# Performance work log

Measured on AMD Instinct MI355X. Metric: run time of the kernel, lower is better.

The kernel has to match this reference:

```python
import jax, jax.numpy as jnp
import numpy as np

N, E, G = 20000, 320000, 64
DIN, H, EF, FC, OUT = 128, 256, 16, 256, 1
BN_EPS = 1e-5


def _gine_layer(x, src, dst, edge_attr, We, be, Wa, ba, g, bt, Wb, bb):
    # GINEConv (eps=0): out = mlp(x + sum_j relu(x_j + lin_edge(e_ij)))
    e = edge_attr @ We.T + be                      # [E, in_ch]
    m = jax.nn.relu(x[src] + e)                    # messages [E, in_ch]
    agg = jax.ops.segment_sum(m, dst, num_segments=x.shape[0])
    h = (x + agg) @ Wa.T + ba                      # Linear
    # BatchNorm1d in eval mode with running_mean=0, running_var=1
    inv = jax.lax.rsqrt(jnp.asarray(1.0 + BN_EPS, h.dtype))
    h = jax.nn.relu(h * inv * g + bt)
    return jax.nn.relu(h @ Wb.T + bb)


def _mean_pool(h, batch, num_graphs):
    sums = jax.ops.segment_sum(h, batch, num_segments=num_graphs)
    cnt = jax.ops.segment_sum(jnp.ones((h.shape[0],), h.dtype), batch, num_segments=num_graphs)
    return sums / jnp.maximum(cnt, 1.0)[:, None]


def setup_inputs() -> dict:
    key = jax.random.key(0)
    ks = iter(jax.random.split(key, 64))

    def nrm(shape, s=0.05):
        return jax.random.normal(next(ks), shape, jnp.float32) * s

    inp = {
        "x": jax.random.normal(next(ks), (N, DIN), jnp.float32),
        "edge_attr": jax.random.normal(next(ks), (E, EF), jnp.float32),
        "src": jax.random.randint(next(ks), (E,), 0, N),
        "dst": jax.random.randint(next(ks), (E,), 0, N),
        "batch": jnp.sort(jax.random.randint(next(ks), (N,), 0, G)),
    }
    dims = [(DIN, H), (H, H), (H, H)]
    for i, (din, h) in enumerate(dims, start=1):
        inp[f"We{i}"] = nrm((din, EF));  inp[f"be{i}"] = jnp.zeros((din,), jnp.float32)
        inp[f"Wa{i}"] = nrm((h, din));  inp[f"ba{i}"] = jnp.zeros((h,), jnp.float32)
        inp[f"g{i}"] = jnp.ones((h,), jnp.float32); inp[f"bt{i}"] = jnp.zeros((h,), jnp.float32)
        inp[f"Wb{i}"] = nrm((h, h));    inp[f"bb{i}"] = jnp.zeros((h,), jnp.float32)
    inp["L1w"] = nrm((FC * 3, H * 3)); inp["L1b"] = jnp.zeros((FC * 3,), jnp.float32)
    inp["L2w"] = nrm((OUT, FC * 3));   inp["L2b"] = jnp.zeros((OUT,), jnp.float32)
    return inp


def reference(x, edge_attr, src, dst, batch,
              We1, be1, Wa1, ba1, g1, bt1, Wb1, bb1,
              We2, be2, Wa2, ba2, g2, bt2, Wb2, bb2,
              We3, be3, Wa3, ba3, g3, bt3, Wb3, bb3,
              L1w, L1b, L2w, L2b):
    h1 = _gine_layer(x,  src, dst, edge_attr, We1, be1, Wa1, ba1, g1, bt1, Wb1, bb1)
    h2 = _gine_layer(h1, src, dst, edge_attr, We2, be2, Wa2, ba2, g2, bt2, Wb2, bb2)
    h3 = _gine_layer(h2, src, dst, edge_attr, We3, be3, Wa3, ba3, g3, bt3, Wb3, bb3)
    p = jnp.concatenate([_mean_pool(h1, batch, G),
                         _mean_pool(h2, batch, G),
                         _mean_pool(h3, batch, G)], axis=1)   # [G, 3H]
    h = jax.nn.relu(p @ L1w.T + L1b)   # dropout is identity (training=False)
    return jax.nn.sigmoid(h @ L2w.T + L2b)
```

## Files before the change

kernel.cpp:

```cpp
#include <hip/hip_runtime.h>
#include <math.h>
#include <stdint.h>

#define N_NODES 20000
#define M_PAD 20032
#define N_EDGES 320000
#define N_GRAPHS 64
#define DIN 128
#define H 256
#define POOL_W 768
#define CHUNK 40
#define NCHUNK (N_EDGES / CHUNK)

typedef __attribute__((ext_vector_type(8))) short bf16x8;
typedef __attribute__((ext_vector_type(4))) float f32x4;
typedef __attribute__((ext_vector_type(4))) unsigned int u32x4;
typedef __attribute__((ext_vector_type(2))) unsigned int u32x2;
typedef _Float16 h2 __attribute__((ext_vector_type(2)));

__device__ __forceinline__ unsigned short f2bf(float f) {
    unsigned u = __builtin_bit_cast(unsigned, f);
    u += 0x7FFFu + ((u >> 16) & 1u);
    return (unsigned short)(u >> 16);
}
__device__ __forceinline__ float bf2f(unsigned short u) {
    return __builtin_bit_cast(float, (unsigned)u << 16);
}
__device__ __forceinline__ unsigned short f2h(float f) {
    const _Float16 h = (_Float16)f;
    return __builtin_bit_cast(unsigned short, h);
}

#if __has_builtin(__builtin_amdgcn_fdot2)
#define DOT2(a, b, c) __builtin_amdgcn_fdot2((a), (b), (c), false)
#else
__device__ __forceinline__ float dot2_fallback(h2 a, h2 b, float c) {
    return fmaf((float)a.x, (float)b.x, fmaf((float)a.y, (float)b.y, c));
}
#define DOT2(a, b, c) dot2_fallback((a), (b), (c))
#endif

struct CvtJob  { const float* s; unsigned short* d; int n4; int mode; };
struct CvtJobs { CvtJob j[12]; };

__global__ __launch_bounds__(256) void cvt_all(CvtJobs jobs)
{
    const CvtJob J = jobs.j[blockIdx.y];
    if (J.mode == 2) {
        const ushort4 z = {0, 0, 0, 0};
        for (int i = blockIdx.x * 256 + threadIdx.x; i < J.n4; i += gridDim.x * 256)
            ((ushort4*)J.d)[i] = z;
        return;
    }
    if (J.mode == 1) {
        for (int i = blockIdx.x * 256 + threadIdx.x; i < J.n4; i += gridDim.x * 256) {
            const float4 v = ((const float4*)J.s)[i];
            ushort4 r;
            r.x = f2h(v.x); r.y = f2h(v.y); r.z = f2h(v.z); r.w = f2h(v.w);
            ((ushort4*)J.d)[i] = r;
        }
        return;
    }
    for (int i = blockIdx.x * 256 + threadIdx.x; i < J.n4; i += gridDim.x * 256) {
        const float4 v = ((const float4*)J.s)[i];
        ushort4 r;
        r.x = f2bf(v.x); r.y = f2bf(v.y); r.z = f2bf(v.z); r.w = f2bf(v.w);
        ((ushort4*)J.d)[i] = r;
    }
}

__global__ __launch_bounds__(256) void hist_kernel(const int* __restrict__ dst,
                                                   int* __restrict__ deg)
{
    const int i = blockIdx.x * 256 + threadIdx.x;
    if (i < N_EDGES) atomicAdd(deg + dst[i], 1);
}

__global__ __launch_bounds__(1024) void scan_kernel(const int* __restrict__ deg,
                                                    int* __restrict__ off,
                                                    int* __restrict__ cur,
                                                    const int* __restrict__ batch,
                                                    int* __restrict__ start)
{
    __shared__ int wsum[16];
    __shared__ int carry;
    const int tid = threadIdx.x, wave = tid >> 6, lane = tid & 63;
    if (tid == 0) carry = 0;
    __syncthreads();
    for (int base = 0; base < N_NODES; base += 1024) {
        const int i = base + tid;
        const int v = (i < N_NODES) ? deg[i] : 0;
        int s = v;
#pragma unroll
        for (int d = 1; d < 64; d <<= 1) {
            const int t = __shfl_up(s, d);
            if (lane >= d) s += t;
        }
        if (lane == 63) wsum[wave] = s;
        __syncthreads();
        if (wave == 0) {
            int t = (lane < 16) ? wsum[lane] : 0;
#pragma unroll
            for (int d = 1; d < 16; d <<= 1) {
                const int u = __shfl_up(t, d);
                if (lane >= d) t += u;
            }
            if (lane < 16) wsum[lane] = t;
        }
        __syncthreads();
        const int wbase = (wave == 0) ? 0 : wsum[wave - 1];
        if (i < N_NODES) {
            const int o = carry + wbase + s - v;
            off[i] = o;
            cur[i] = o;
        }
        const int tot = wsum[15];
        __syncthreads();
        if (tid == 0) carry += tot;
        __syncthreads();
    }
    if (tid == 0) off[N_NODES] = carry;

    if (tid <= N_GRAPHS) {
        if (tid == N_GRAPHS) { start[N_GRAPHS] = N_NODES; }
        else {
            int lo = 0, hi = N_NODES;
            while (lo < hi) { const int mid = (lo + hi) >> 1; if (batch[mid] < tid) lo = mid + 1; else hi = mid; }
            start[tid] = lo;
        }
    }
}

__global__ __launch_bounds__(256) void chunkmap_kernel(const int* __restrict__ off,
                                                       int* __restrict__ cmap)
{
    const int w = blockIdx.x * 256 + threadIdx.x;
    if (w > NCHUNK) return;
    if (w == NCHUNK) { cmap[w] = N_NODES; return; }
    const int target = w * CHUNK;
    int lo = 0, hi = N_NODES;
    while (lo < hi) { const int mid = (lo + hi) >> 1; if (off[mid] < target) lo = mid + 1; else hi = mid; }
    cmap[w] = lo;
}

__global__ __launch_bounds__(256) void scatter_kernel(
    const int* __restrict__ src, const int* __restrict__ dst,
    const float* __restrict__ ea, int* __restrict__ cursor,
    int* __restrict__ ssrc, unsigned short* __restrict__ eas)
{
    const int e = blockIdx.x * 256 + threadIdx.x;
    if (e < N_EDGES) {
        const int p = atomicAdd(cursor + dst[e], 1);
        ssrc[p] = src[e];
        const float4* er = (const float4*)(ea + (size_t)e * 16);
        unsigned short* dr = eas + (size_t)p * 16;
        ushort4* d4 = (ushort4*)dr;
#pragma unroll
        for (int q = 0; q < 4; ++q) {
            const float4 v = er[q];
            ushort4 r;
            r.x = f2h(v.x); r.y = f2h(v.y); r.z = f2h(v.z); r.w = f2h(v.w);
            d4[q] = r;
        }
    }
}

template<int IN>
__global__ __launch_bounds__(256) void agg3(
    const unsigned short* __restrict__ xb,
    const unsigned short* __restrict__ eas,
    const int* __restrict__ ssrc,
    const int* __restrict__ off,
    const int* __restrict__ cmap,
    const unsigned short* __restrict__ Weh,
    const float* __restrict__ be,
    unsigned short* __restrict__ out)
{
    constexpr int CPL = IN / 64;
    constexpr int XW  = CPL / 2;
    const int lane = threadIdx.x & 63;
    const int wid  = blockIdx.x * 4 + (threadIdx.x >> 6);
    const int c0 = lane * CPL;
    const int zd = __builtin_amdgcn_mbcnt_lo(0u, 0u);

    u32x4 wlo[CPL], whi[CPL];
    float bias[CPL], acc[CPL];
#pragma unroll
    for (int j = 0; j < CPL; ++j) {
        const u32x4* wr = (const u32x4*)(Weh + (size_t)(c0 + j) * 16);
        wlo[j] = wr[0];
        whi[j] = wr[1];
        bias[j] = be[c0 + j];
        acc[j]  = 0.0f;
    }
#pragma unroll
    for (int j = 0; j < CPL; ++j) {
#pragma unroll
        for (int k = 0; k < 4; ++k) {
            { float t = __builtin_bit_cast(float, wlo[j][k]); asm volatile("" : "+v"(t)); wlo[j][k] = __builtin_bit_cast(unsigned int, t); }
            { float t = __builtin_bit_cast(float, whi[j][k]); asm volatile("" : "+v"(t)); whi[j][k] = __builtin_bit_cast(unsigned int, t); }
        }
        asm volatile("" : "+v"(bias[j]));
    }

    int n          = __builtin_amdgcn_readfirstlane(cmap[wid]);
    const int nend = __builtin_amdgcn_readfirstlane(cmap[wid + 1]);
    if (n >= nend) return;
    int p          = __builtin_amdgcn_readfirstlane(off[n]);
    const int pend = __builtin_amdgcn_readfirstlane(off[nend]);

    auto ldx = [&](int s) -> u32x2 {
        if constexpr (XW == 2) {
            return *(const u32x2*)(xb + (size_t)s * IN + c0);
        } else {
            u32x2 r;
            r[0] = *(const unsigned int*)(xb + (size_t)s * IN + c0);
            r[1] = 0u;
            return r;
        }
    };
    auto flushv = [&](int nn, u32x2 xs) {
        if constexpr (XW == 2) {
            const float x0 = __builtin_bit_cast(float, xs[0] << 16);
            const float x1 = __builtin_bit_cast(float, xs[0] & 0xFFFF0000u);
            const float x2 = __builtin_bit_cast(float, xs[1] << 16);
            const float x3 = __builtin_bit_cast(float, xs[1] & 0xFFFF0000u);
            u32x2 o;
            o[0] = (unsigned)f2bf(x0 + acc[0]) | ((unsigned)f2bf(x1 + acc[1]) << 16);
            o[1] = (unsigned)f2bf(x2 + acc[2]) | ((unsigned)f2bf(x3 + acc[3]) << 16);
            *(u32x2*)(out + (size_t)nn * IN + c0) = o;
        } else {
            const float x0 = __builtin_bit_cast(float, xs[0] << 16);
            const float x1 = __builtin_bit_cast(float, xs[0] & 0xFFFF0000u);
            const unsigned int o =
                (unsigned)f2bf(x0 + acc[0]) | ((unsigned)f2bf(x1 + acc[1]) << 16);
            *(unsigned int*)(out + (size_t)nn * IN + c0) = o;
        }
#pragma unroll
        for (int j = 0; j < CPL; ++j) acc[j] = 0.0f;
    };

    int p1 = __builtin_amdgcn_readfirstlane(off[n + 1]);
    while (p1 == p) {
        flushv(n, ldx(n)); ++n;
        if (n >= nend) return;
        p1 = __builtin_amdgcn_readfirstlane(off[n + 1]);
    }
    u32x2 xself = ldx(n);

    auto ldeL = [&](int q) -> u32x4 {
        return ((const u32x4*)(eas + (size_t)(q + zd) * 16))[0];
    };
    auto ldeH = [&](int q) -> u32x4 {
        return ((const u32x4*)(eas + (size_t)(q + zd) * 16))[1];
    };
    auto ldsrc = [&](int q) -> int {
        const int qc = (q < N_EDGES) ? q : (N_EDGES - 1);
        return ssrc[qc + zd];
    };
    auto edge_compute = [&](u32x4 eL, u32x4 eH, u32x2 xw) {
        float m[CPL];
#pragma unroll
        for (int j = 0; j < CPL; ++j) m[j] = bias[j];
#pragma unroll
        for (int k = 0; k < 4; ++k) {
            const h2 ep = __builtin_bit_cast(h2, eL[k]);
#pragma unroll
            for (int j = 0; j < CPL; ++j)
                m[j] = DOT2(ep, __builtin_bit_cast(h2, wlo[j][k]), m[j]);
        }
#pragma unroll
        for (int k = 0; k < 4; ++k) {
            const h2 ep = __builtin_bit_cast(h2, eH[k]);
#pragma unroll
            for (int j = 0; j < CPL; ++j)
                m[j] = DOT2(ep, __builtin_bit_cast(h2, whi[j][k]), m[j]);
        }
#pragma unroll
        for (int j = 0; j < CPL; ++j) {
            const unsigned int word = xw[j >> 1];
            const float xf = __builtin_bit_cast(float,
                (j & 1) ? (word & 0xFFFF0000u) : (word << 16));
            acc[j] += fmaxf(m[j] + xf, 0.0f);
        }
    };
    auto adv = [&]() {
        flushv(n, xself); ++n;
        while (n < nend) {
            p1 = __builtin_amdgcn_readfirstlane(off[n + 1]);
            if (p1 != p) { xself = ldx(n); break; }
            flushv(n, ldx(n)); ++n;
        }
    };

    int sA = ldsrc(p),     sB = ldsrc(p + 1), sC = ldsrc(p + 2), sD = ldsrc(p + 3);
    u32x4 eLA = ldeL(p),     eHA = ldeH(p);
    u32x4 eLB = ldeL(p + 1), eHB = ldeH(p + 1);
    u32x4 eLC = ldeL(p + 2), eHC = ldeH(p + 2);
    u32x4 eLD = ldeL(p + 3), eHD = ldeH(p + 3);
    u32x2 xA = ldx(sA), xB = ldx(sB), xC = ldx(sC), xD = ldx(sD);
    sA = ldsrc(p + 4); sB = ldsrc(p + 5); sC = ldsrc(p + 6); sD = ldsrc(p + 7);

    for (;;) {
        edge_compute(eLA, eHA, xA);
        eLA = ldeL(p + 4); eHA = ldeH(p + 4); xA = ldx(sA); sA = ldsrc(p + 8);
        ++p; if (p == p1) adv();
        if (p >= pend) break;

        edge_compute(eLB, eHB, xB);
        eLB = ldeL(p + 4); eHB = ldeH(p + 4); xB = ldx(sB); sB = ldsrc(p + 8);
        ++p; if (p == p1) adv();
        if (p >= pend) break;

        edge_compute(eLC, eHC, xC);
        eLC = ldeL(p + 4); eHC = ldeH(p + 4); xC = ldx(sC); sC = ldsrc(p + 8);
        ++p; if (p == p1) adv();
        if (p >= pend) break;

        edge_compute(eLD, eHD, xD);
        eLD = ldeL(p + 4); eHD = ldeH(p + 4); xD = ldx(sD); sD = ldsrc(p + 8);
        ++p; if (p == p1) adv();
        if (p >= pend) break;
    }
    while (n < nend) { flushv(n, ldx(n)); ++n; }
}

template<int K, int EPI>
__global__ __launch_bounds__(256) void gemm_ldsA(
    const unsigned short* __restrict__ A,
    const unsigned short* __restrict__ W,
    const float* __restrict__ bias,
    const float* __restrict__ gsc, const float* __restrict__ bsh,
    unsigned short* __restrict__ out)
{
    constexpr int KC = K / 32;
    constexpr int SLOTS = K / 8;
    __shared__ unsigned short Al[64 * K];

    const int w = threadIdx.x >> 6, lane = threadIdx.x & 63;
    const int lm = lane & 15, lq = lane >> 4;
    const int n0 = (blockIdx.y * 4 + w) * 32;
    const int m0 = blockIdx.x * 64;

#pragma unroll
    for (int i = 0; i < 64 * SLOTS / 256; ++i) {
        const int t = i * 256 + threadIdx.x;
        const int row = t / SLOTS, slot = t % SLOTS;
        const uint4 v = *(const uint4*)(A + (size_t)(m0 + row) * K + slot * 8);
        *(uint4*)((char*)Al + row * (K * 2) + ((slot ^ (row & 7)) * 16)) = v;
    }

    bf16x8 B0[KC], B1[KC];
    {
        const unsigned short* Wp0 = W + (size_t)(n0 + lm) * K + lq * 8;
        const unsigned short* Wp1 = W + (size_t)(n0 + 16 + lm) * K + lq * 8;
#pragma unroll
        for (int c = 0; c < KC; ++c) {
            B0[c] = *(const bf16x8*)(Wp0 + c * 32);
            B1[c] = *(const bf16x8*)(Wp1 + c * 32);
        }
    }

    const float inv = rsqrtf(1.0f + 1e-5f);
    const float bc0 = bias[n0 + lm],      bc1 = bias[n0 + 16 + lm];
    const float gc0 = (EPI == 0) ? gsc[n0 + lm]      : 0.0f;
    const float gc1 = (EPI == 0) ? gsc[n0 + 16 + lm] : 0.0f;
    const float sc0 = (EPI == 0) ? bsh[n0 + lm]      : 0.0f;
    const float sc1 = (EPI == 0) ? bsh[n0 + 16 + lm] : 0.0f;

    __syncthreads();

#pragma unroll
    for (int ch = 0; ch < 4; ++ch) {
        const int row = ch * 16 + lm;
        const char* rbase = (const char*)Al + row * (K * 2);
        bf16x8 aC[KC];
#pragma unroll
        for (int c = 0; c < KC; ++c) {
            const int slot = (lq + c * 4) ^ (row & 7);
            aC[c] = *(const bf16x8*)(rbase + slot * 16);
        }

        f32x4 acc0 = (f32x4){0.f, 0.f, 0.f, 0.f};
        f32x4 acc1 = (f32x4){0.f, 0.f, 0.f, 0.f};
#pragma unroll
        for (int c = 0; c < KC; ++c) {
            acc0 = __builtin_amdgcn_mfma_f32_16x16x32_bf16(aC[c], B0[c], acc0, 0, 0, 0);
            acc1 = __builtin_amdgcn_mfma_f32_16x16x32_bf16(aC[c], B1[c], acc1, 0, 0, 0);
        }

        const int mr = m0 + ch * 16;
#pragma unroll
        for (int r = 0; r < 4; ++r) {
            const int rowo = mr + lq * 4 + r;
            if (EPI == 1 && rowo >= N_NODES) continue;
            float v0 = acc0[r] + bc0;
            float v1 = acc1[r] + bc1;
            if (EPI == 0) {
                v0 = fmaxf(v0 * inv * gc0 + sc0, 0.0f);
                v1 = fmaxf(v1 * inv * gc1 + sc1, 0.0f);
            } else {
                v0 = fmaxf(v0, 0.0f);
                v1 = fmaxf(v1, 0.0f);
            }
            out[(size_t)rowo * H + n0 + lm]      = f2bf(v0);
            out[(size_t)rowo * H + n0 + 16 + lm] = f2bf(v1);
        }
    }
}

#define RSPLIT 6
__global__ __launch_bounds__(256) void pool2(
    const unsigned short* __restrict__ h1, const unsigned short* __restrict__ h2,
    const unsigned short* __restrict__ h3, const int* __restrict__ start,
    float* __restrict__ pool)
{
    const int g = blockIdx.x & 63, layer = blockIdx.x >> 6;
    const unsigned short* h = (layer == 0) ? h1 : (layer == 1) ? h2 : h3;
    const int r0 = start[g], r1 = start[g + 1];
    const int nr = r1 - r0;
    if (nr <= 0) return;
    const int chunk = (nr + RSPLIT - 1) / RSPLIT;
    const int rs = r0 + blockIdx.y * chunk;
    const int re = (rs + chunk < r1) ? rs + chunk : r1;
    if (rs >= re) return;

    const int c = threadIdx.x;
    float s0 = 0.f, s1 = 0.f, s2 = 0.f, s3 = 0.f;
    int r = rs;
    for (; r + 4 <= re; r += 4) {
        s0 += bf2f(h[(size_t)(r + 0) * H + c]);
        s1 += bf2f(h[(size_t)(r + 1) * H + c]);
        s2 += bf2f(h[(size_t)(r + 2) * H + c]);
        s3 += bf2f(h[(size_t)(r + 3) * H + c]);
    }
    for (; r < re; ++r) s0 += bf2f(h[(size_t)r * H + c]);
    atomicAdd(&pool[(size_t)g * POOL_W + layer * 256 + c], s0 + s1 + s2 + s3);
}

__global__ __launch_bounds__(256) void fc_head(
    const float* __restrict__ pool, const int* __restrict__ start,
    const float* __restrict__ L1w, const float* __restrict__ L1b,
    const float* __restrict__ L2w, float* __restrict__ gsum)
{
    const int g = blockIdx.x;
    __shared__ float p[POOL_W];

    const float rc = 1.0f / fmaxf((float)(start[g + 1] - start[g]), 1.0f);
    for (int i = threadIdx.x; i < POOL_W; i += 256)
        p[i] = pool[(size_t)g * POOL_W + i] * rc;
    __syncthreads();

    const int wv = threadIdx.x >> 6, lane = threadIdx.x & 63;
    const float4* p4 = (const float4*)p;
    const float4 pa = p4[lane], pb = p4[lane + 64], pc = p4[lane + 128];

    const int ob = blockIdx.y * 64 + wv * 16;
    float part = 0.0f;
#pragma unroll 4
    for (int t = 0; t < 16; ++t) {
        const int o = ob + t;
        const float4* wr = (const float4*)(L1w + (size_t)o * POOL_W);
        const float4 a = wr[lane], b = wr[lane + 64], c = wr[lane + 128];
        float acc = a.x * pa.x + a.y * pa.y + a.z * pa.z + a.w * pa.w
                  + b.x * pb.x + b.y * pb.y + b.z * pb.z + b.w * pb.w
                  + c.x * pc.x + c.y * pc.y + c.z * pc.z + c.w * pc.w;
#pragma unroll
        for (int off = 32; off > 0; off >>= 1) acc += __shfl_xor(acc, off);
        if (lane == 0) part += fmaxf(acc + L1b[o], 0.0f) * L2w[o];
    }
    if (lane == 0) atomicAdd(&gsum[g], part);
}

__global__ __launch_bounds__(64) void sig_kernel(
    const float* __restrict__ gsum, const float* __restrict__ L2b,
    float* __restrict__ out)
{
    const int g = threadIdx.x;
    if (g < N_GRAPHS) out[g] = 1.0f / (1.0f + expf(-(gsum[g] + L2b[0])));
}

extern "C" void kernel_launch(void* const* d_in, const int* in_sizes, int n_in,
                              void* d_out, int out_size, void* d_ws, size_t ws_size,
                              hipStream_t stream)
{
    const float* x     = (const float*)d_in[0];
    const float* ea    = (const float*)d_in[1];
    const int*   src   = (const int*)d_in[2];
    const int*   dst   = (const int*)d_in[3];
    const int*   batch = (const int*)d_in[4];

    const float* We[3]; const float* be[3]; const float* Wa[3]; const float* ba[3];
    const float* gg[3]; const float* bt[3]; const float* Wb[3]; const float* bb[3];
    for (int l = 0; l < 3; ++l) {
        const int o = 5 + 8 * l;
        We[l] = (const float*)d_in[o + 0]; be[l] = (const float*)d_in[o + 1];
        Wa[l] = (const float*)d_in[o + 2]; ba[l] = (const float*)d_in[o + 3];
        gg[l] = (const float*)d_in[o + 4]; bt[l] = (const float*)d_in[o + 5];
        Wb[l] = (const float*)d_in[o + 6]; bb[l] = (const float*)d_in[o + 7];
    }
    const float* L1w = (const float*)d_in[29];
    const float* L1b = (const float*)d_in[30];
    const float* L2w = (const float*)d_in[31];
    const float* L2b = (const float*)d_in[32];

    float* pool   = (float*)d_ws;
    float* gsum   = pool + (size_t)N_GRAPHS * POOL_W;
    int*   deg    = (int*)(gsum + N_GRAPHS);
    int*   off    = deg + N_NODES;
    int*   cursor = off + N_NODES + 1;
    int*   start  = cursor + N_NODES;
    int*   cmap   = start + 72;
    int*   ssrc   = (int*)((((uintptr_t)(cmap + NCHUNK + 1)) + 31) & ~(uintptr_t)31);
    unsigned short* eas = (unsigned short*)((((uintptr_t)(ssrc + N_EDGES + 16)) + 31) & ~(uintptr_t)31);
    unsigned short* xb = (unsigned short*)((((uintptr_t)(eas + (size_t)(N_EDGES + 16) * 16)) + 31) & ~(uintptr_t)31);
    unsigned short* u  = xb + (size_t)M_PAD * DIN;
    unsigned short* tT = u  + (size_t)M_PAD * H;
    unsigned short* h1 = tT + (size_t)M_PAD * H;
    unsigned short* h2 = h1 + (size_t)M_PAD * H;
    unsigned short* h3 = h2 + (size_t)M_PAD * H;
    unsigned short* wbf[6];
    wbf[0] = h3 + (size_t)M_PAD * H;
    wbf[1] = wbf[0] + H * DIN;
    for (int i = 2; i < 6; ++i) wbf[i] = wbf[i - 1] + H * H;
    unsigned short* weh[3];
    weh[0] = wbf[5] + H * H;
    weh[1] = weh[0] + DIN * 16;
    weh[2] = weh[1] + H * 16;

    CvtJobs jobs;
    jobs.j[0]  = { x,       xb,                    N_NODES * DIN / 4,       0 };
    jobs.j[1]  = { Wa[0],   wbf[0],                H * DIN / 4,             0 };
    jobs.j[2]  = { Wb[0],   wbf[1],                H * H / 4,               0 };
    jobs.j[3]  = { Wa[1],   wbf[2],                H * H / 4,               0 };
    jobs.j[4]  = { Wb[1],   wbf[3],                H * H / 4,               0 };
    jobs.j[5]  = { Wa[2],   wbf[4],                H * H / 4,               0 };
    jobs.j[6]  = { Wb[2],   wbf[5],                H * H / 4,               0 };
    jobs.j[7]  = { nullptr, (unsigned short*)deg,  N_NODES * 4 / 8,         2 };
    jobs.j[8]  = { nullptr, (unsigned short*)pool, (N_GRAPHS * POOL_W + N_GRAPHS) * 4 / 8, 2 };
    jobs.j[9]  = { We[0],   weh[0],                DIN * 16 / 4,            1 };
    jobs.j[10] = { We[1],   weh[1],                H * 16 / 4,              1 };
    jobs.j[11] = { We[2],   weh[2],                H * 16 / 4,              1 };
    cvt_all<<<dim3(320, 12), 256, 0, stream>>>(jobs);

    hist_kernel<<<(N_EDGES + 255) / 256, 256, 0, stream>>>(dst, deg);
    scan_kernel<<<1, 1024, 0, stream>>>(deg, off, cursor, batch, start);
    chunkmap_kernel<<<(NCHUNK + 256) / 256, 256, 0, stream>>>(off, cmap);
    scatter_kernel<<<(N_EDGES + 255) / 256, 256, 0, stream>>>(src, dst, ea, cursor, ssrc, eas);

    const int  agrid = NCHUNK / 4;
    const dim3 ggrid(M_PAD / 64, 2);

    agg3<DIN><<<agrid, 256, 0, stream>>>(xb, eas, ssrc, off, cmap, weh[0], be[0], u);
    gemm_ldsA<DIN, 0><<<ggrid, 256, 0, stream>>>(u, wbf[0], ba[0], gg[0], bt[0], tT);
    gemm_ldsA<H,   1><<<ggrid, 256, 0, stream>>>(tT, wbf[1], bb[0], nullptr, nullptr, h1);
    agg3<H><<<agrid, 256, 0, stream>>>(h1, eas, ssrc, off, cmap, weh[1], be[1], u);
    gemm_ldsA<H, 0><<<ggrid, 256, 0, stream>>>(u, wbf[2], ba[1], gg[1], bt[1], tT);
    gemm_ldsA<H, 1><<<ggrid, 256, 0, stream>>>(tT, wbf[3], bb[1], nullptr, nullptr, h2);
    agg3<H><<<agrid, 256, 0, stream>>>(h2, eas, ssrc, off, cmap, weh[2], be[2], u);
    gemm_ldsA<H, 0><<<ggrid, 256, 0, stream>>>(u, wbf[4], ba[2], gg[2], bt[2], tT);
    gemm_ldsA<H, 1><<<ggrid, 256, 0, stream>>>(tT, wbf[5], bb[2], nullptr, nullptr, h3);

    pool2<<<dim3(3 * N_GRAPHS, RSPLIT), 256, 0, stream>>>(h1, h2, h3, start, pool);
    fc_head<<<dim3(N_GRAPHS, POOL_W / 64), 256, 0, stream>>>(pool, start, L1w, L1b, L2w, gsum);
    sig_kernel<<<1, 64, 0, stream>>>(gsum, L2b, (float*)d_out);
}
```

Baseline: 481.2 us.

## Fuse the two MLP GEMMs per layer through LDS and fold chunkmap into scan

Each layer's Linear-BN-ReLU GEMM and following Linear-ReLU GEMM are merged into one 512-thread kernel. The intermediate 64x256 tile stays in swizzled LDS instead of round-tripping through global memory. The chunk-map binary search moves into the single-block scan kernel, removing one launch, and agg3 gets an occupancy hint via launch bounds. In exchange the fused kernel uses more LDS per block, which limits occupancy, and the chunkmap work now runs serially on one block.

Result: slower. 498.2 us (+3.5%).

```diff
diff --git a/kernel.cpp b/kernel.cpp
--- a/kernel.cpp
+++ b/kernel.cpp
@@ -80,7 +80,8 @@
                                                     int* __restrict__ off,
                                                     int* __restrict__ cur,
                                                     const int* __restrict__ batch,
-                                                    int* __restrict__ start)
+                                                    int* __restrict__ start,
+                                                    int* __restrict__ cmap)
 {
     __shared__ int wsum[16];
     __shared__ int carry;
@@ -120,6 +121,7 @@
         __syncthreads();
     }
     if (tid == 0) off[N_NODES] = carry;
+    __syncthreads();
 
     if (tid <= N_GRAPHS) {
         if (tid == N_GRAPHS) { start[N_GRAPHS] = N_NODES; }
@@ -129,18 +131,13 @@
             start[tid] = lo;
         }
     }
-}
-
-__global__ __launch_bounds__(256) void chunkmap_kernel(const int* __restrict__ off,
-                                                       int* __restrict__ cmap)
-{
-    const int w = blockIdx.x * 256 + threadIdx.x;
-    if (w > NCHUNK) return;
-    if (w == NCHUNK) { cmap[w] = N_NODES; return; }
-    const int target = w * CHUNK;
-    int lo = 0, hi = N_NODES;
-    while (lo < hi) { const int mid = (lo + hi) >> 1; if (off[mid] < target) lo = mid + 1; else hi = mid; }
-    cmap[w] = lo;
+    for (int w = tid; w <= NCHUNK; w += 1024) {
+        if (w == NCHUNK) { cmap[w] = N_NODES; continue; }
+        const int target = w * CHUNK;
+        int lo = 0, hi = N_NODES;
+        while (lo < hi) { const int mid = (lo + hi) >> 1; if (off[mid] < target) lo = mid + 1; else hi = mid; }
+        cmap[w] = lo;
+    }
 }
 
 __global__ __launch_bounds__(256) void scatter_kernel(
@@ -166,7 +163,7 @@
 }
 
 template<int IN>
-__global__ __launch_bounds__(256) void agg3(
+__global__ __launch_bounds__(256, 4) void agg3(
     const unsigned short* __restrict__ xb,
     const unsigned short* __restrict__ eas,
     const int* __restrict__ ssrc,
@@ -325,48 +322,50 @@
     while (n < nend) { flushv(n, ldx(n)); ++n; }
 }
 
-template<int K, int EPI>
-__global__ __launch_bounds__(256) void gemm_ldsA(
+template<int K>
+__global__ __launch_bounds__(512, 2) void gemm_fused(
     const unsigned short* __restrict__ A,
-    const unsigned short* __restrict__ W,
-    const float* __restrict__ bias,
+    const unsigned short* __restrict__ Wa,
+    const float* __restrict__ ba,
     const float* __restrict__ gsc, const float* __restrict__ bsh,
+    const unsigned short* __restrict__ Wb,
+    const float* __restrict__ bb,
     unsigned short* __restrict__ out)
 {
-    constexpr int KC = K / 32;
+    constexpr int KC1 = K / 32;
+    constexpr int KC2 = H / 32;
     constexpr int SLOTS = K / 8;
     __shared__ unsigned short Al[64 * K];
+    __shared__ unsigned short Tl[64 * H];
 
     const int w = threadIdx.x >> 6, lane = threadIdx.x & 63;
     const int lm = lane & 15, lq = lane >> 4;
-    const int n0 = (blockIdx.y * 4 + w) * 32;
+    const int n0 = w * 32;
     const int m0 = blockIdx.x * 64;
 
 #pragma unroll
-    for (int i = 0; i < 64 * SLOTS / 256; ++i) {
-        const int t = i * 256 + threadIdx.x;
+    for (int i = 0; i < 64 * SLOTS / 512; ++i) {
+        const int t = i * 512 + threadIdx.x;
         const int row = t / SLOTS, slot = t % SLOTS;
         const uint4 v = *(const uint4*)(A + (size_t)(m0 + row) * K + slot * 8);
         *(uint4*)((char*)Al + row * (K * 2) + ((slot ^ (row & 7)) * 16)) = v;
     }
 
-    bf16x8 B0[KC], B1[KC];
+    bf16x8 B0[KC2], B1[KC2];
     {
-        const unsigned short* Wp0 = W + (size_t)(n0 + lm) * K + lq * 8;
-        const unsigned short* Wp1 = W + (size_t)(n0 + 16 + lm) * K + lq * 8;
-#pragma unroll
-        for (int c = 0; c < KC; ++c) {
+        const unsigned short* Wp0 = Wa + (size_t)(n0 + lm) * K + lq * 8;
+        const unsigned short* Wp1 = Wa + (size_t)(n0 + 16 + lm) * K + lq * 8;
+#pragma unroll
+        for (int c = 0; c < KC1; ++c) {
             B0[c] = *(const bf16x8*)(Wp0 + c * 32);
             B1[c] = *(const bf16x8*)(Wp1 + c * 32);
         }
     }
 
     const float inv = rsqrtf(1.0f + 1e-5f);
-    const float bc0 = bias[n0 + lm],      bc1 = bias[n0 + 16 + lm];
-    const float gc0 = (EPI == 0) ? gsc[n0 + lm]      : 0.0f;
-    const float gc1 = (EPI == 0) ? gsc[n0 + 16 + lm] : 0.0f;
-    const float sc0 = (EPI == 0) ? bsh[n0 + lm]      : 0.0f;
-    const float sc1 = (EPI == 0) ? bsh[n0 + 16 + lm] : 0.0f;
+    const float bc0 = ba[n0 + lm],  bc1 = ba[n0 + 16 + lm];
+    const float gc0 = gsc[n0 + lm], gc1 = gsc[n0 + 16 + lm];
+    const float sc0 = bsh[n0 + lm], sc1 = bsh[n0 + 16 + lm];
 
     __syncthreads();
 
@@ -374,35 +373,69 @@
     for (int ch = 0; ch < 4; ++ch) {
         const int row = ch * 16 + lm;
         const char* rbase = (const char*)Al + row * (K * 2);
-        bf16x8 aC[KC];
-#pragma unroll
-        for (int c = 0; c < KC; ++c) {
+        bf16x8 aC[KC1];
+#pragma unroll
+        for (int c = 0; c < KC1; ++c) {
             const int slot = (lq + c * 4) ^ (row & 7);
             aC[c] = *(const bf16x8*)(rbase + slot * 16);
         }
-
         f32x4 acc0 = (f32x4){0.f, 0.f, 0.f, 0.f};
         f32x4 acc1 = (f32x4){0.f, 0.f, 0.f, 0.f};
 #pragma unroll
-        for (int c = 0; c < KC; ++c) {
+        for (int c = 0; c < KC1; ++c) {
             acc0 = __builtin_amdgcn_mfma_f32_16x16x32_bf16(aC[c], B0[c], acc0, 0, 0, 0);
             acc1 = __builtin_amdgcn_mfma_f32_16x16x32_bf16(aC[c], B1[c], acc1, 0, 0, 0);
         }
-
+#pragma unroll
+        for (int r = 0; r < 4; ++r) {
+            const int rowo = ch * 16 + lq * 4 + r;
+            const float v0 = fmaxf((acc0[r] + bc0) * inv * gc0 + sc0, 0.0f);
+            const float v1 = fmaxf((acc1[r] + bc1) * inv * gc1 + sc1, 0.0f);
+            const int col0 = n0 + lm, col1 = n0 + 16 + lm;
+            *(unsigned short*)((char*)Tl + rowo * (H * 2)
+                + (((col0 >> 3) ^ (rowo & 7)) << 4) + ((col0 & 7) << 1)) = f2bf(v0);
+            *(unsigned short*)((char*)Tl + rowo * (H * 2)
+                + (((col1 >> 3) ^ (rowo & 7)) << 4) + ((col1 & 7) << 1)) = f2bf(v1);
+        }
+    }
+
+    {
+        const unsigned short* Wp0 = Wb + (size_t)(n0 + lm) * H + lq * 8;
+        const unsigned short* Wp1 = Wb + (size_t)(n0 + 16 + lm) * H + lq * 8;
+#pragma unroll
+        for (int c = 0; c < KC2; ++c) {
+            B0[c] = *(const bf16x8*)(Wp0 + c * 32);
+            B1[c] = *(const bf16x8*)(Wp1 + c * 32);
+        }
+    }
+    const float eb0 = bb[n0 + lm], eb1 = bb[n0 + 16 + lm];
+
+    __syncthreads();
+
+#pragma unroll
+    for (int ch = 0; ch < 4; ++ch) {
+        const int row = ch * 16 + lm;
+        const char* rbase = (const char*)Tl + row * (H * 2);
+        bf16x8 aC[KC2];
+#pragma unroll
+        for (int c = 0; c < KC2; ++c) {
+            const int slot = (lq + c * 4) ^ (row & 7);
+            aC[c] = *(const bf16x8*)(rbase + slot * 16);
+        }
+        f32x4 acc0 = (f32x4){0.f, 0.f, 0.f, 0.f};
+        f32x4 acc1 = (f32x4){0.f, 0.f, 0.f, 0.f};
+#pragma unroll
+        for (int c = 0; c < KC2; ++c) {
+            acc0 = __builtin_amdgcn_mfma_f32_16x16x32_bf16(aC[c], B0[c], acc0, 0, 0, 0);
+            acc1 = __builtin_amdgcn_mfma_f32_16x16x32_bf16(aC[c], B1[c], acc1, 0, 0, 0);
+        }
         const int mr = m0 + ch * 16;
 #pragma unroll
         for (int r = 0; r < 4; ++r) {
             const int rowo = mr + lq * 4 + r;
-            if (EPI == 1 && rowo >= N_NODES) continue;
-            float v0 = acc0[r] + bc0;
-            float v1 = acc1[r] + bc1;
-            if (EPI == 0) {
-                v0 = fmaxf(v0 * inv * gc0 + sc0, 0.0f);
-                v1 = fmaxf(v1 * inv * gc1 + sc1, 0.0f);
-            } else {
-                v0 = fmaxf(v0, 0.0f);
-                v1 = fmaxf(v1, 0.0f);
-            }
+            if (rowo >= N_NODES) continue;
+            const float v0 = fmaxf(acc0[r] + eb0, 0.0f);
+            const float v1 = fmaxf(acc1[r] + eb1, 0.0f);
             out[(size_t)rowo * H + n0 + lm]      = f2bf(v0);
             out[(size_t)rowo * H + n0 + 16 + lm] = f2bf(v1);
         }
@@ -515,8 +548,7 @@
     unsigned short* eas = (unsigned short*)((((uintptr_t)(ssrc + N_EDGES + 16)) + 31) & ~(uintptr_t)31);
     unsigned short* xb = (unsigned short*)((((uintptr_t)(eas + (size_t)(N_EDGES + 16) * 16)) + 31) & ~(uintptr_t)31);
     unsigned short* u  = xb + (size_t)M_PAD * DIN;
-    unsigned short* tT = u  + (size_t)M_PAD * H;
-    unsigned short* h1 = tT + (size_t)M_PAD * H;
+    unsigned short* h1 = u  + (size_t)M_PAD * H;
     unsigned short* h2 = h1 + (size_t)M_PAD * H;
     unsigned short* h3 = h2 + (size_t)M_PAD * H;
     unsigned short* wbf[6];
@@ -544,22 +576,18 @@
     cvt_all<<<dim3(320, 12), 256, 0, stream>>>(jobs);
 
     hist_kernel<<<(N_EDGES + 255) / 256, 256, 0, stream>>>(dst, deg);
-    scan_kernel<<<1, 1024, 0, stream>>>(deg, off, cursor, batch, start);
-    chunkmap_kernel<<<(NCHUNK + 256) / 256, 256, 0, stream>>>(off, cmap);
+    scan_kernel<<<1, 1024, 0, stream>>>(deg, off, cursor, batch, start, cmap);
     scatter_kernel<<<(N_EDGES + 255) / 256, 256, 0, stream>>>(src, dst, ea, cursor, ssrc, eas);
 
-    const int  agrid = NCHUNK / 4;
-    const dim3 ggrid(M_PAD / 64, 2);
+    const int agrid = NCHUNK / 4;
+    const int ggrid = M_PAD / 64;
 
     agg3<DIN><<<agrid, 256, 0, stream>>>(xb, eas, ssrc, off, cmap, weh[0], be[0], u);
-    gemm_ldsA<DIN, 0><<<ggrid, 256, 0, stream>>>(u, wbf[0], ba[0], gg[0], bt[0], tT);
-    gemm_ldsA<H,   1><<<ggrid, 256, 0, stream>>>(tT, wbf[1], bb[0], nullptr, nullptr, h1);
+    gemm_fused<DIN><<<ggrid, 512, 0, stream>>>(u, wbf[0], ba[0], gg[0], bt[0], wbf[1], bb[0], h1);
     agg3<H><<<agrid, 256, 0, stream>>>(h1, eas, ssrc, off, cmap, weh[1], be[1], u);
-    gemm_ldsA<H, 0><<<ggrid, 256, 0, stream>>>(u, wbf[2], ba[1], gg[1], bt[1], tT);
-    gemm_ldsA<H, 1><<<ggrid, 256, 0, stream>>>(tT, wbf[3], bb[1], nullptr, nullptr, h2);
+    gemm_fused<H><<<ggrid, 512, 0, stream>>>(u, wbf[2], ba[1], gg[1], bt[1], wbf[3], bb[1], h2);
     agg3<H><<<agrid, 256, 0, stream>>>(h2, eas, ssrc, off, cmap, weh[2], be[2], u);
-    gemm_ldsA<H, 0><<<ggrid, 256, 0, stream>>>(u, wbf[4], ba[2], gg[2], bt[2], tT);
-    gemm_ldsA<H, 1><<<ggrid, 256, 0, stream>>>(tT, wbf[5], bb[2], nullptr, nullptr, h3);
+    gemm_fused<H><<<ggrid, 512, 0, stream>>>(u, wbf[4], ba[2], gg[2], bt[2], wbf[5], bb[2], h3);
 
     pool2<<<dim3(3 * N_GRAPHS, RSPLIT), 256, 0, stream>>>(h1, h2, h3, start, pool);
     fc_head<<<dim3(N_GRAPHS, POOL_W / 64), 256, 0, stream>>>(pool, start, L1w, L1b, L2w, gsum);
```
